# Kernel tuning notes

Measured on AMD Instinct MI355X. Metric: run time of the kernel, lower is better.

The kernel has to match this reference:

```python
import jax, jax.numpy as jnp
import numpy as np

N = 100000   # num_nodes
E = 300000   # num_edges
R = 200      # num_rels
B = 32       # num_bases (bdd blocks)
H = 128      # h_dim
SI = H // B  # submat_in = 4


def setup_inputs() -> dict:
    key = jax.random.key(0)
    ks = jax.random.split(key, 10)
    return {
        "node_ids": jnp.arange(N, dtype=jnp.int32),
        "src": jax.random.randint(ks[0], (E,), 0, N, dtype=jnp.int32),
        "dst": jax.random.randint(ks[1], (E,), 0, N, dtype=jnp.int32),
        "etypes": jax.random.randint(ks[2], (E,), 0, R, dtype=jnp.int32),
        "norm": jax.random.uniform(ks[3], (E, 1), dtype=jnp.float32),
        "emb": jax.random.normal(ks[4], (N, H), dtype=jnp.float32) * 0.02,
        "W1": jax.random.normal(ks[5], (R, B, SI, SI), dtype=jnp.float32) / np.float32(np.sqrt(SI)),
        "loop_w1": jax.random.normal(ks[6], (H, H), dtype=jnp.float32) / np.float32(np.sqrt(H)),
        "bias1": jnp.zeros((H,), dtype=jnp.float32),
        "W2": jax.random.normal(ks[7], (R, B, SI, 2 * SI), dtype=jnp.float32) / np.float32(np.sqrt(SI)),
        "loop_w2": jax.random.normal(ks[8], (H, 2 * H), dtype=jnp.float32) / np.float32(np.sqrt(H)),
        "bias2": jnp.zeros((2 * H,), dtype=jnp.float32),
        "eps": jax.random.normal(ks[9], (N, H), dtype=jnp.float32),
    }


def rel_graph_conv_bdd(h, src, dst, etypes, norm, W, loop_w, bias):
    """DGL RelGraphConv with regularizer='bdd', self_loop=True, bias=True."""
    _, Bb, si, so = W.shape
    h_src = h[src].reshape(-1, Bb, si)                  # (E, B, si)
    We = W[etypes]                                      # (E, B, si, so) gathered block weights
    msg = jnp.einsum('ebi,ebio->ebo', h_src, We).reshape(-1, Bb * so)  # (E, out)
    msg = msg * norm                                    # edge norm
    agg = jax.ops.segment_sum(msg, dst, num_segments=N)  # scatter-add to dst
    return agg + bias + h @ loop_w


def reference(node_ids, src, dst, etypes, norm, emb, W1, loop_w1, bias1, W2, loop_w2, bias2, eps):
    h = emb[node_ids]                                   # embedding lookup (N, H)
    h = jax.nn.relu(rel_graph_conv_bdd(h, src, dst, etypes, norm, W1, loop_w1, bias1))
    h = rel_graph_conv_bdd(h, src, dst, etypes, norm, W2, loop_w2, bias2)  # (N, 2H)
    # utils.gaussian_parameters: split last dim, v = softplus + 1e-8
    m, h_pre = jnp.split(h, 2, axis=-1)
    v = jax.nn.softplus(h_pre) + 1e-8
    # utils.sample_gaussian: reparameterized sample
    z = m + jnp.sqrt(v) * eps
    return z
```

## Files before the change

kernel.cpp:

```cpp
#include <hip/hip_runtime.h>
#include <math.h>

#define HD 128

union F4 { float4 v; float f[4]; };

typedef __attribute__((ext_vector_type(8))) short bf8_t;
typedef __attribute__((ext_vector_type(4))) float f4_t;

__device__ __forceinline__ float dot4(const F4& a, const F4& b){
  return fmaf(a.f[0], b.f[0], fmaf(a.f[1], b.f[1], fmaf(a.f[2], b.f[2], a.f[3]*b.f[3])));
}

__device__ __forceinline__ unsigned short f2bf(float f){
  unsigned int u = __float_as_uint(f);
  return (unsigned short)((u + 0x7fffu + ((u>>16)&1u)) >> 16);
}

__global__ void k_count(const int* __restrict__ dst, int* __restrict__ counts, int E){
  int e = blockIdx.x*256 + threadIdx.x;
  if (e < E) atomicAdd(&counts[dst[e]], 1);
}

__global__ void k_scan_block(const int* __restrict__ counts, int* __restrict__ scanTmp,
                             int* __restrict__ blockSums, int n){
  __shared__ int sm[256];
  int i = blockIdx.x*256 + threadIdx.x;
  int v = (i<n)?counts[i]:0;
  sm[threadIdx.x]=v; __syncthreads();
  for (int ofs=1; ofs<256; ofs<<=1){
    int t = (threadIdx.x>=ofs)?sm[threadIdx.x-ofs]:0;
    __syncthreads();
    sm[threadIdx.x]+=t;
    __syncthreads();
  }
  if (i<n) scanTmp[i]=sm[threadIdx.x];
  if (threadIdx.x==255) blockSums[blockIdx.x]=sm[255];
}

__global__ void k_scan_top(int* __restrict__ blockSums, int nb){
  __shared__ int sm[1024];
  int v = ((int)threadIdx.x<nb)?blockSums[threadIdx.x]:0;
  sm[threadIdx.x]=v; __syncthreads();
  for (int ofs=1; ofs<1024; ofs<<=1){
    int t = ((int)threadIdx.x>=ofs)?sm[threadIdx.x-ofs]:0;
    __syncthreads();
    sm[threadIdx.x]+=t;
    __syncthreads();
  }
  if ((int)threadIdx.x<nb) blockSums[threadIdx.x] = sm[threadIdx.x]-v;
}

__global__ void k_scan_fin(const int* __restrict__ scanTmp, const int* __restrict__ blockSums,
                           const int* __restrict__ counts,
                           int* __restrict__ row_ptr, int* __restrict__ cursors, int n){
  int i = blockIdx.x*256 + threadIdx.x;
  if (i<n){
    int incl = scanTmp[i] + blockSums[blockIdx.x];
    row_ptr[i+1] = incl;
    cursors[i] = incl - counts[i];
  }
  if (i==0) row_ptr[0]=0;
}

__global__ void k_scatter(const int* __restrict__ dst, const int* __restrict__ src,
                          const int* __restrict__ et, const float* __restrict__ norm,
                          int* __restrict__ cursors, int4* __restrict__ pay, int E){
  int e = blockIdx.x*256 + threadIdx.x;
  if (e<E){
    int p = atomicAdd(&cursors[dst[e]],1);
    pay[p] = make_int4(src[e], et[e], __float_as_int(norm[e]), 0);
  }
}

__global__ void k_w1t(const float* __restrict__ W, float* __restrict__ WT, int n){
  int d = blockIdx.x*256 + threadIdx.x;
  if (d < n){
    int i = d & 3, o = (d>>2) & 3, rb = d>>4;
    WT[d] = W[rb*16 + i*4 + o];
  }
}
__global__ void k_w2t(const float* __restrict__ W, float* __restrict__ WT, int n){
  int d = blockIdx.x*256 + threadIdx.x;
  if (d < n){
    int i = d & 3, o = (d>>2) & 7, rb = d>>5;
    WT[d] = W[rb*32 + i*8 + o];
  }
}

__global__ void k_wpack(const float* __restrict__ W, unsigned short* __restrict__ Wp,
                        int NCT, int NO){
  int t = blockIdx.x*256 + threadIdx.x;
  if (t >= NCT*256) return;
  int lane = t & 63, ks = (t>>6) & 3, ct = t >> 8;
  int k0 = ks*32 + (lane>>4)*8, col = ct*16 + (lane&15);
  unsigned short v[8];
  #pragma unroll
  for (int j=0;j<8;++j) v[j] = f2bf(W[(k0+j)*NO + col]);
  ushort4* dst = (ushort4*)&Wp[(size_t)t*8];
  dst[0] = make_ushort4(v[0],v[1],v[2],v[3]);
  dst[1] = make_ushort4(v[4],v[5],v[6],v[7]);
}

__global__ void k_gather(const int* __restrict__ ids, const float4* __restrict__ emb4,
                         float4* __restrict__ h0, unsigned short* __restrict__ h0b, int nf4){
  int i = blockIdx.x*256+threadIdx.x;
  if (i<nf4){
    int row = i>>5, c = i&31;
    float4 v = emb4[ids[row]*32 + c];
    h0[i] = v;
    *(ushort4*)&h0b[(size_t)i*4] = make_ushort4(f2bf(v.x),f2bf(v.y),f2bf(v.z),f2bf(v.w));
  }
}

__global__ __launch_bounds__(256)
void k_edge1(const int* __restrict__ row_ptr, const int4* __restrict__ pay,
             const float* __restrict__ h, const float* __restrict__ WT,
             float* __restrict__ agg, int Nn){
  int wid = (blockIdx.x*256 + threadIdx.x)>>6;
  wid = __builtin_amdgcn_readfirstlane(wid);
  int lane = threadIdx.x & 63;
  if (wid >= Nn) return;
  int e0 = row_ptr[wid], e1 = row_ptr[wid+1];
  int b0 = lane>>2, o = lane&3;
  float acc0=0.f, acc1=0.f;
  for (int e=e0; e<e1; e+=2){
    int4 p0 = pay[e];
    bool has2 = (e+1 < e1);
    int4 p1 = has2 ? pay[e+1] : p0;
    float n0 = __int_as_float(p0.z);
    float n1 = has2 ? __int_as_float(p1.z) : 0.f;
    const float* ha = &h[p0.x*HD];  const float* wa = &WT[p0.y*512];
    const float* hb = &h[p1.x*HD];  const float* wb = &WT[p1.y*512];
    F4 hA0,hB0,wA0,wB0,hA1,hB1,wA1,wB1;
    hA0.v = *(const float4*)&ha[b0*4];
    hB0.v = *(const float4*)&ha[(b0+16)*4];
    wA0.v = *(const float4*)&wa[b0*16 + o*4];
    wB0.v = *(const float4*)&wa[(b0+16)*16 + o*4];
    hA1.v = *(const float4*)&hb[b0*4];
    hB1.v = *(const float4*)&hb[(b0+16)*4];
    wA1.v = *(const float4*)&wb[b0*16 + o*4];
    wB1.v = *(const float4*)&wb[(b0+16)*16 + o*4];
    acc0 = fmaf(n0, dot4(hA0,wA0), acc0);
    acc1 = fmaf(n0, dot4(hB0,wB0), acc1);
    acc0 = fmaf(n1, dot4(hA1,wA1), acc0);
    acc1 = fmaf(n1, dot4(hB1,wB1), acc1);
  }
  agg[wid*HD + lane]      = acc0;
  agg[wid*HD + 64 + lane] = acc1;
}

__global__ __launch_bounds__(256)
void k_edge2(const int* __restrict__ row_ptr, const int4* __restrict__ pay,
             const float* __restrict__ h, const float* __restrict__ WT,
             float* __restrict__ agg, int Nn){
  int wid = (blockIdx.x*256 + threadIdx.x)>>6;
  wid = __builtin_amdgcn_readfirstlane(wid);
  int lane = threadIdx.x & 63;
  if (wid >= Nn) return;
  int e0 = row_ptr[wid], e1 = row_ptr[wid+1];
  int ob = lane>>3, o = lane&7;
  float acc[4] = {0.f,0.f,0.f,0.f};
  for (int e=e0; e<e1; e+=2){
    int4 p0 = pay[e];
    bool has2 = (e+1 < e1);
    int4 p1 = has2 ? pay[e+1] : p0;
    float n0 = __int_as_float(p0.z);
    float n1 = has2 ? __int_as_float(p1.z) : 0.f;
    const float* ha = &h[p0.x*HD];  const float* wa = &WT[p0.y*1024];
    const float* hb = &h[p1.x*HD];  const float* wb = &WT[p1.y*1024];
    F4 hva[4], wva[4], hvb[4], wvb[4];
    #pragma unroll
    for (int u=0; u<4; ++u){
      int b = ob + 8*u;
      hva[u].v = *(const float4*)&ha[b*4];
      wva[u].v = *(const float4*)&wa[b*32 + o*4];
      hvb[u].v = *(const float4*)&hb[b*4];
      wvb[u].v = *(const float4*)&wb[b*32 + o*4];
    }
    #pragma unroll
    for (int u=0; u<4; ++u){
      acc[u] = fmaf(n0, dot4(hva[u],wva[u]), acc[u]);
      acc[u] = fmaf(n1, dot4(hvb[u],wvb[u]), acc[u]);
    }
  }
  #pragma unroll
  for (int u=0; u<4; ++u) agg[wid*256 + u*64 + lane] = acc[u];
}

__global__ __launch_bounds__(256)
void k_mfma_relu(const unsigned short* __restrict__ Ab, const unsigned short* __restrict__ Wp,
                 const float* __restrict__ agg, const float* __restrict__ bias,
                 float* __restrict__ out, unsigned short* __restrict__ outb, int M){
  const int lane = threadIdx.x & 63;
  const int rowBase = blockIdx.x*64 + (threadIdx.x>>6)*16;
  const int ar = lane & 15, kg = lane >> 4;
  const int aclamp = min(rowBase + ar, M-1);
  f4_t acc[8];
  #pragma unroll
  for (int ct=0; ct<8; ++ct) acc[ct] = (f4_t)0.f;
  #pragma unroll
  for (int ks=0; ks<4; ++ks){
    bf8_t a = *(const bf8_t*)&Ab[(size_t)aclamp*HD + ks*32 + kg*8];
    #pragma unroll
    for (int ct=0; ct<8; ++ct){
      bf8_t b = *(const bf8_t*)&Wp[(size_t)((ct*4 + ks)*64 + lane)*8];
      acc[ct] = __builtin_amdgcn_mfma_f32_16x16x32_bf16(a, b, acc[ct], 0,0,0);
    }
  }
  const int crow = rowBase + kg*4;
  #pragma unroll
  for (int r=0; r<4; ++r){
    int gr = crow + r;
    if (gr >= M) continue;
    #pragma unroll
    for (int ct=0; ct<8; ++ct){
      int col = ct*16 + ar;
      float v = fmaxf(acc[ct][r] + agg[(size_t)gr*128 + col] + bias[col], 0.f);
      out[(size_t)gr*128 + col] = v;
      outb[(size_t)gr*128 + col] = f2bf(v);
    }
  }
}

__global__ __launch_bounds__(256)
void k_mfma_gauss(const unsigned short* __restrict__ Ab, const unsigned short* __restrict__ Wp,
                  const float* __restrict__ agg, const float* __restrict__ bias,
                  const float* __restrict__ eps, float* __restrict__ out, int M){
  const int lane = threadIdx.x & 63;
  const int bx = blockIdx.x & 1;
  const int rowBase = (blockIdx.x>>1)*64 + (threadIdx.x>>6)*16;
  const int ar = lane & 15, kg = lane >> 4;
  const int aclamp = min(rowBase + ar, M-1);
  f4_t accm[4], acch[4];
  #pragma unroll
  for (int ct=0; ct<4; ++ct){ accm[ct] = (f4_t)0.f; acch[ct] = (f4_t)0.f; }
  #pragma unroll
  for (int ks=0; ks<4; ++ks){
    bf8_t a = *(const bf8_t*)&Ab[(size_t)aclamp*HD + ks*32 + kg*8];
    #pragma unroll
    for (int ct=0; ct<4; ++ct){
      int ctm = bx*4 + ct, cth = 8 + bx*4 + ct;
      bf8_t bm = *(const bf8_t*)&Wp[(size_t)((ctm*4 + ks)*64 + lane)*8];
      bf8_t bh = *(const bf8_t*)&Wp[(size_t)((cth*4 + ks)*64 + lane)*8];
      accm[ct] = __builtin_amdgcn_mfma_f32_16x16x32_bf16(a, bm, accm[ct], 0,0,0);
      acch[ct] = __builtin_amdgcn_mfma_f32_16x16x32_bf16(a, bh, acch[ct], 0,0,0);
    }
  }
  const int crow = rowBase + kg*4;
  #pragma unroll
  for (int r=0; r<4; ++r){
    int gr = crow + r;
    if (gr >= M) continue;
    #pragma unroll
    for (int ct=0; ct<4; ++ct){
      int colm = bx*64 + ct*16 + ar;
      float m  = accm[ct][r] + agg[(size_t)gr*256 + colm]       + bias[colm];
      float hp = acch[ct][r] + agg[(size_t)gr*256 + colm + 128] + bias[colm+128];
      float sp = fmaxf(hp, 0.f) + log1pf(expf(-fabsf(hp)));
      out[(size_t)gr*128 + colm] = fmaf(sqrtf(sp + 1e-8f), eps[(size_t)gr*128 + colm], m);
    }
  }
}

extern "C" void kernel_launch(void* const* d_in, const int* in_sizes, int n_in,
                              void* d_out, int out_size, void* d_ws, size_t ws_size,
                              hipStream_t stream){
  (void)n_in; (void)out_size; (void)ws_size;
  const int*   node_ids = (const int*)d_in[0];
  const int*   src  = (const int*)d_in[1];
  const int*   dst  = (const int*)d_in[2];
  const int*   et   = (const int*)d_in[3];
  const float* norm = (const float*)d_in[4];
  const float* emb  = (const float*)d_in[5];
  const float* W1   = (const float*)d_in[6];
  const float* lw1  = (const float*)d_in[7];
  const float* b1   = (const float*)d_in[8];
  const float* W2   = (const float*)d_in[9];
  const float* lw2  = (const float*)d_in[10];
  const float* b2   = (const float*)d_in[11];
  const float* eps  = (const float*)d_in[12];
  float* out = (float*)d_out;

  const int N  = in_sizes[0];
  const int E  = in_sizes[1];
  const int n1 = in_sizes[6];
  const int n2 = in_sizes[9];

  char* w = (char*)d_ws;
  size_t szNH = (size_t)N*HD*sizeof(float);
  float* h0   = (float*)(w);
  float* agg2 = (float*)(w);
  float* h1   = (float*)(w + 2*szNH);
  float* agg1 = (float*)(w + 3*szNH);
  char*  ip   = w + 4*szNH;
  int4*  pay       = (int4*)ip;
  int*   counts    = (int*)(pay + E);
  int*   scanTmp   = counts + N;
  int*   row_ptr   = scanTmp + N;
  int*   cursors   = row_ptr + (N+1);
  int*   blockSums = cursors + N;
  float* W1T       = (float*)(blockSums + 1024);
  float* W2T       = W1T + n1;
  size_t tail      = ((size_t)((char*)(W2T + n2) - w) + 63) & ~(size_t)63;
  unsigned short* W1p = (unsigned short*)(w + tail);
  unsigned short* W2p = W1p + 8*256*8;
  unsigned short* h0b = W2p + 16*256*8;
  unsigned short* h1b = h0b + (size_t)N*HD;

  hipMemsetAsync(counts, 0, (size_t)N*sizeof(int), stream);

  int nb_e    = (E+255)/256;
  int nb_scan = (N+255)/256;

  k_w1t<<<(n1+255)/256, 256, 0, stream>>>(W1, W1T, n1);
  k_w2t<<<(n2+255)/256, 256, 0, stream>>>(W2, W2T, n2);
  k_wpack<<<8, 256, 0, stream>>>(lw1, W1p, 8, 128);
  k_wpack<<<16, 256, 0, stream>>>(lw2, W2p, 16, 256);
  k_gather<<<(N*32+255)/256, 256, 0, stream>>>(node_ids, (const float4*)emb, (float4*)h0, h0b, N*32);
  k_count<<<nb_e, 256, 0, stream>>>(dst, counts, E);
  k_scan_block<<<nb_scan, 256, 0, stream>>>(counts, scanTmp, blockSums, N);
  k_scan_top<<<1, 1024, 0, stream>>>(blockSums, nb_scan);
  k_scan_fin<<<nb_scan, 256, 0, stream>>>(scanTmp, blockSums, counts, row_ptr, cursors, N);
  k_scatter<<<nb_e, 256, 0, stream>>>(dst, src, et, norm, cursors, pay, E);

  int nb_rows = (N+3)/4;
  int nb_m    = (N+63)/64;

  k_edge1<<<nb_rows, 256, 0, stream>>>(row_ptr, pay, h0, W1T, agg1, N);
  k_mfma_relu<<<nb_m, 256, 0, stream>>>(h0b, W1p, agg1, b1, h1, h1b, N);
  k_edge2<<<nb_rows, 256, 0, stream>>>(row_ptr, pay, h1, W2T, agg2, N);
  k_mfma_gauss<<<nb_m*2, 256, 0, stream>>>(h1b, W2p, agg2, b2, eps, out, N);
}
```

Baseline: 430.5 us.

## Fuse prep kernels, store relation weights in bf16, remap edge kernels per block

Merges the embedding gather, in-degree count, per-relation weight transposes and self-loop weight packing into one launch, cutting five kernel launches. The per-relation block-diagonal weights are now stored as bf16, halving weight gather traffic in the edge kernels. The edge kernels are remapped so each lane owns one 4-wide input block and computes all of that block's outputs. The two half-wavefronts take alternate edges, with one payload prefetched ahead, and their partial sums are merged by a cross-half shuffle before a vectorized store. The bf16 weights add rounding error to the message computation, and the new mapping leaves half the lanes idle on nodes with a single in-edge.

```diff
diff --git a/kernel.cpp b/kernel.cpp
--- a/kernel.cpp
+++ b/kernel.cpp
@@ -7,19 +7,66 @@
 
 typedef __attribute__((ext_vector_type(8))) short bf8_t;
 typedef __attribute__((ext_vector_type(4))) float f4_t;
-
-__device__ __forceinline__ float dot4(const F4& a, const F4& b){
-  return fmaf(a.f[0], b.f[0], fmaf(a.f[1], b.f[1], fmaf(a.f[2], b.f[2], a.f[3]*b.f[3])));
-}
 
 __device__ __forceinline__ unsigned short f2bf(float f){
   unsigned int u = __float_as_uint(f);
   return (unsigned short)((u + 0x7fffu + ((u>>16)&1u)) >> 16);
 }
 
-__global__ void k_count(const int* __restrict__ dst, int* __restrict__ counts, int E){
-  int e = blockIdx.x*256 + threadIdx.x;
-  if (e < E) atomicAdd(&counts[dst[e]], 1);
+__device__ __forceinline__ float dotbf(const F4& h, unsigned int ua, unsigned int ub){
+  float w0 = __uint_as_float(ua << 16);
+  float w1 = __uint_as_float(ua & 0xffff0000u);
+  float w2 = __uint_as_float(ub << 16);
+  float w3 = __uint_as_float(ub & 0xffff0000u);
+  return fmaf(h.f[0], w0, fmaf(h.f[1], w1, fmaf(h.f[2], w2, h.f[3]*w3)));
+}
+
+__device__ __forceinline__ void wpack_one(const float* __restrict__ W,
+                                          unsigned short* __restrict__ Wp, int t, int NO){
+  int lane = t & 63, ks = (t>>6) & 3, ct = t >> 8;
+  int k0 = ks*32 + (lane>>4)*8, col = ct*16 + (lane&15);
+  unsigned short v[8];
+  #pragma unroll
+  for (int j=0;j<8;++j) v[j] = f2bf(W[(k0+j)*NO + col]);
+  ushort4* dst = (ushort4*)&Wp[(size_t)t*8];
+  dst[0] = make_ushort4(v[0],v[1],v[2],v[3]);
+  dst[1] = make_ushort4(v[4],v[5],v[6],v[7]);
+}
+
+__global__ void k_prep(const int* __restrict__ ids, const float4* __restrict__ emb4,
+                       float4* __restrict__ h0, unsigned short* __restrict__ h0b,
+                       const int* __restrict__ dst, int* __restrict__ counts,
+                       const float* __restrict__ W1, unsigned short* __restrict__ W1Tb,
+                       const float* __restrict__ W2, unsigned short* __restrict__ W2Tb,
+                       const float* __restrict__ lw1, unsigned short* __restrict__ W1p,
+                       const float* __restrict__ lw2, unsigned short* __restrict__ W2p,
+                       int NG, int E, int n1, int n2){
+  int i = blockIdx.x*256 + threadIdx.x;
+  if (i < NG){
+    int row = i>>5, c = i&31;
+    float4 v = emb4[ids[row]*32 + c];
+    h0[i] = v;
+    *(ushort4*)&h0b[(size_t)i*4] = make_ushort4(f2bf(v.x),f2bf(v.y),f2bf(v.z),f2bf(v.w));
+    return;
+  }
+  i -= NG;
+  if (i < E){ atomicAdd(&counts[dst[i]], 1); return; }
+  i -= E;
+  if (i < n1){
+    int ii = i & 3, o = (i>>2) & 3, rb = i>>4;
+    W1Tb[i] = f2bf(W1[rb*16 + ii*4 + o]);
+    return;
+  }
+  i -= n1;
+  if (i < n2){
+    int ii = i & 3, o = (i>>2) & 7, rb = i>>5;
+    W2Tb[i] = f2bf(W2[rb*32 + ii*8 + o]);
+    return;
+  }
+  i -= n2;
+  if (i < 2048){ wpack_one(lw1, W1p, i, 128); return; }
+  i -= 2048;
+  if (i < 4096){ wpack_one(lw2, W2p, i, 256); }
 }
 
 __global__ void k_scan_block(const int* __restrict__ counts, int* __restrict__ scanTmp,
@@ -73,119 +120,79 @@
   }
 }
 
-__global__ void k_w1t(const float* __restrict__ W, float* __restrict__ WT, int n){
-  int d = blockIdx.x*256 + threadIdx.x;
-  if (d < n){
-    int i = d & 3, o = (d>>2) & 3, rb = d>>4;
-    WT[d] = W[rb*16 + i*4 + o];
-  }
-}
-__global__ void k_w2t(const float* __restrict__ W, float* __restrict__ WT, int n){
-  int d = blockIdx.x*256 + threadIdx.x;
-  if (d < n){
-    int i = d & 3, o = (d>>2) & 7, rb = d>>5;
-    WT[d] = W[rb*32 + i*8 + o];
-  }
-}
-
-__global__ void k_wpack(const float* __restrict__ W, unsigned short* __restrict__ Wp,
-                        int NCT, int NO){
-  int t = blockIdx.x*256 + threadIdx.x;
-  if (t >= NCT*256) return;
-  int lane = t & 63, ks = (t>>6) & 3, ct = t >> 8;
-  int k0 = ks*32 + (lane>>4)*8, col = ct*16 + (lane&15);
-  unsigned short v[8];
-  #pragma unroll
-  for (int j=0;j<8;++j) v[j] = f2bf(W[(k0+j)*NO + col]);
-  ushort4* dst = (ushort4*)&Wp[(size_t)t*8];
-  dst[0] = make_ushort4(v[0],v[1],v[2],v[3]);
-  dst[1] = make_ushort4(v[4],v[5],v[6],v[7]);
-}
-
-__global__ void k_gather(const int* __restrict__ ids, const float4* __restrict__ emb4,
-                         float4* __restrict__ h0, unsigned short* __restrict__ h0b, int nf4){
-  int i = blockIdx.x*256+threadIdx.x;
-  if (i<nf4){
-    int row = i>>5, c = i&31;
-    float4 v = emb4[ids[row]*32 + c];
-    h0[i] = v;
-    *(ushort4*)&h0b[(size_t)i*4] = make_ushort4(f2bf(v.x),f2bf(v.y),f2bf(v.z),f2bf(v.w));
-  }
-}
-
 __global__ __launch_bounds__(256)
 void k_edge1(const int* __restrict__ row_ptr, const int4* __restrict__ pay,
-             const float* __restrict__ h, const float* __restrict__ WT,
+             const float* __restrict__ h, const unsigned short* __restrict__ WTb,
              float* __restrict__ agg, int Nn){
-  int wid = (blockIdx.x*256 + threadIdx.x)>>6;
-  wid = __builtin_amdgcn_readfirstlane(wid);
-  int lane = threadIdx.x & 63;
+  int wid = __builtin_amdgcn_readfirstlane((blockIdx.x*256 + threadIdx.x)>>6);
   if (wid >= Nn) return;
-  int e0 = row_ptr[wid], e1 = row_ptr[wid+1];
-  int b0 = lane>>2, o = lane&3;
-  float acc0=0.f, acc1=0.f;
-  for (int e=e0; e<e1; e+=2){
-    int4 p0 = pay[e];
-    bool has2 = (e+1 < e1);
-    int4 p1 = has2 ? pay[e+1] : p0;
-    float n0 = __int_as_float(p0.z);
-    float n1 = has2 ? __int_as_float(p1.z) : 0.f;
-    const float* ha = &h[p0.x*HD];  const float* wa = &WT[p0.y*512];
-    const float* hb = &h[p1.x*HD];  const float* wb = &WT[p1.y*512];
-    F4 hA0,hB0,wA0,wB0,hA1,hB1,wA1,wB1;
-    hA0.v = *(const float4*)&ha[b0*4];
-    hB0.v = *(const float4*)&ha[(b0+16)*4];
-    wA0.v = *(const float4*)&wa[b0*16 + o*4];
-    wB0.v = *(const float4*)&wa[(b0+16)*16 + o*4];
-    hA1.v = *(const float4*)&hb[b0*4];
-    hB1.v = *(const float4*)&hb[(b0+16)*4];
-    wA1.v = *(const float4*)&wb[b0*16 + o*4];
-    wB1.v = *(const float4*)&wb[(b0+16)*16 + o*4];
-    acc0 = fmaf(n0, dot4(hA0,wA0), acc0);
-    acc1 = fmaf(n0, dot4(hB0,wB0), acc1);
-    acc0 = fmaf(n1, dot4(hA1,wA1), acc0);
-    acc1 = fmaf(n1, dot4(hB1,wB1), acc1);
-  }
-  agg[wid*HD + lane]      = acc0;
-  agg[wid*HD + 64 + lane] = acc1;
+  const int lane = threadIdx.x & 63;
+  const int half = lane >> 5, b = lane & 31;
+  const int e0 = row_ptr[wid], e1 = row_ptr[wid+1];
+  float a0=0.f, a1=0.f, a2=0.f, a3=0.f;
+  int e = e0 + half;
+  int4 p;
+  if (e < e1) p = pay[e];
+  for (; e < e1; e += 2){
+    int4 pn = (e+2 < e1) ? pay[e+2] : p;
+    float nm = __int_as_float(p.z);
+    F4 hv; hv.v = *(const float4*)&h[(size_t)p.x*HD + b*4];
+    const uint4* wq = (const uint4*)&WTb[(size_t)p.y*512 + b*16];
+    uint4 q0 = wq[0], q1 = wq[1];
+    a0 = fmaf(nm, dotbf(hv, q0.x, q0.y), a0);
+    a1 = fmaf(nm, dotbf(hv, q0.z, q0.w), a1);
+    a2 = fmaf(nm, dotbf(hv, q1.x, q1.y), a2);
+    a3 = fmaf(nm, dotbf(hv, q1.z, q1.w), a3);
+    p = pn;
+  }
+  a0 += __shfl_xor(a0, 32); a1 += __shfl_xor(a1, 32);
+  a2 += __shfl_xor(a2, 32); a3 += __shfl_xor(a3, 32);
+  if (half == 0){
+    F4 o; o.f[0]=a0; o.f[1]=a1; o.f[2]=a2; o.f[3]=a3;
+    *(float4*)&agg[(size_t)wid*128 + b*4] = o.v;
+  }
 }
 
 __global__ __launch_bounds__(256)
 void k_edge2(const int* __restrict__ row_ptr, const int4* __restrict__ pay,
-             const float* __restrict__ h, const float* __restrict__ WT,
+             const float* __restrict__ h, const unsigned short* __restrict__ WTb,
              float* __restrict__ agg, int Nn){
-  int wid = (blockIdx.x*256 + threadIdx.x)>>6;
-  wid = __builtin_amdgcn_readfirstlane(wid);
-  int lane = threadIdx.x & 63;
+  int wid = __builtin_amdgcn_readfirstlane((blockIdx.x*256 + threadIdx.x)>>6);
   if (wid >= Nn) return;
-  int e0 = row_ptr[wid], e1 = row_ptr[wid+1];
-  int ob = lane>>3, o = lane&7;
-  float acc[4] = {0.f,0.f,0.f,0.f};
-  for (int e=e0; e<e1; e+=2){
-    int4 p0 = pay[e];
-    bool has2 = (e+1 < e1);
-    int4 p1 = has2 ? pay[e+1] : p0;
-    float n0 = __int_as_float(p0.z);
-    float n1 = has2 ? __int_as_float(p1.z) : 0.f;
-    const float* ha = &h[p0.x*HD];  const float* wa = &WT[p0.y*1024];
-    const float* hb = &h[p1.x*HD];  const float* wb = &WT[p1.y*1024];
-    F4 hva[4], wva[4], hvb[4], wvb[4];
-    #pragma unroll
-    for (int u=0; u<4; ++u){
-      int b = ob + 8*u;
-      hva[u].v = *(const float4*)&ha[b*4];
-      wva[u].v = *(const float4*)&wa[b*32 + o*4];
-      hvb[u].v = *(const float4*)&hb[b*4];
-      wvb[u].v = *(const float4*)&wb[b*32 + o*4];
-    }
-    #pragma unroll
-    for (int u=0; u<4; ++u){
-      acc[u] = fmaf(n0, dot4(hva[u],wva[u]), acc[u]);
-      acc[u] = fmaf(n1, dot4(hvb[u],wvb[u]), acc[u]);
-    }
-  }
-  #pragma unroll
-  for (int u=0; u<4; ++u) agg[wid*256 + u*64 + lane] = acc[u];
+  const int lane = threadIdx.x & 63;
+  const int half = lane >> 5, b = lane & 31;
+  const int e0 = row_ptr[wid], e1 = row_ptr[wid+1];
+  float acc[8];
+  #pragma unroll
+  for (int o=0;o<8;++o) acc[o]=0.f;
+  int e = e0 + half;
+  int4 p;
+  if (e < e1) p = pay[e];
+  for (; e < e1; e += 2){
+    int4 pn = (e+2 < e1) ? pay[e+2] : p;
+    float nm = __int_as_float(p.z);
+    F4 hv; hv.v = *(const float4*)&h[(size_t)p.x*HD + b*4];
+    const uint4* wq = (const uint4*)&WTb[(size_t)p.y*1024 + b*32];
+    uint4 q0 = wq[0], q1 = wq[1], q2 = wq[2], q3 = wq[3];
+    acc[0] = fmaf(nm, dotbf(hv, q0.x, q0.y), acc[0]);
+    acc[1] = fmaf(nm, dotbf(hv, q0.z, q0.w), acc[1]);
+    acc[2] = fmaf(nm, dotbf(hv, q1.x, q1.y), acc[2]);
+    acc[3] = fmaf(nm, dotbf(hv, q1.z, q1.w), acc[3]);
+    acc[4] = fmaf(nm, dotbf(hv, q2.x, q2.y), acc[4]);
+    acc[5] = fmaf(nm, dotbf(hv, q2.z, q2.w), acc[5]);
+    acc[6] = fmaf(nm, dotbf(hv, q3.x, q3.y), acc[6]);
+    acc[7] = fmaf(nm, dotbf(hv, q3.z, q3.w), acc[7]);
+    p = pn;
+  }
+  #pragma unroll
+  for (int o=0;o<8;++o) acc[o] += __shfl_xor(acc[o], 32);
+  if (half == 0){
+    F4 o0, o1;
+    #pragma unroll
+    for (int j=0;j<4;++j){ o0.f[j]=acc[j]; o1.f[j]=acc[4+j]; }
+    *(float4*)&agg[(size_t)wid*256 + b*8]     = o0.v;
+    *(float4*)&agg[(size_t)wid*256 + b*8 + 4] = o1.v;
+  }
 }
 
 __global__ __launch_bounds__(256)
@@ -300,25 +307,24 @@
   int*   row_ptr   = scanTmp + N;
   int*   cursors   = row_ptr + (N+1);
   int*   blockSums = cursors + N;
-  float* W1T       = (float*)(blockSums + 1024);
-  float* W2T       = W1T + n1;
-  size_t tail      = ((size_t)((char*)(W2T + n2) - w) + 63) & ~(size_t)63;
-  unsigned short* W1p = (unsigned short*)(w + tail);
-  unsigned short* W2p = W1p + 8*256*8;
-  unsigned short* h0b = W2p + 16*256*8;
-  unsigned short* h1b = h0b + (size_t)N*HD;
+  size_t tail      = ((size_t)((char*)(blockSums + 1024) - w) + 63) & ~(size_t)63;
+  unsigned short* W1Tb = (unsigned short*)(w + tail);
+  unsigned short* W2Tb = W1Tb + n1;
+  unsigned short* W1p  = W2Tb + n2;
+  unsigned short* W2p  = W1p + 8*256*8;
+  unsigned short* h0b  = W2p + 16*256*8;
+  unsigned short* h1b  = h0b + (size_t)N*HD;
 
   hipMemsetAsync(counts, 0, (size_t)N*sizeof(int), stream);
 
+  const int NG = N*32;
+  const int Tprep = NG + E + n1 + n2 + 2048 + 4096;
   int nb_e    = (E+255)/256;
   int nb_scan = (N+255)/256;
 
-  k_w1t<<<(n1+255)/256, 256, 0, stream>>>(W1, W1T, n1);
-  k_w2t<<<(n2+255)/256, 256, 0, stream>>>(W2, W2T, n2);
-  k_wpack<<<8, 256, 0, stream>>>(lw1, W1p, 8, 128);
-  k_wpack<<<16, 256, 0, stream>>>(lw2, W2p, 16, 256);
-  k_gather<<<(N*32+255)/256, 256, 0, stream>>>(node_ids, (const float4*)emb, (float4*)h0, h0b, N*32);
-  k_count<<<nb_e, 256, 0, stream>>>(dst, counts, E);
+  k_prep<<<(Tprep+255)/256, 256, 0, stream>>>(node_ids, (const float4*)emb, (float4*)h0, h0b,
+                                              dst, counts, W1, W1Tb, W2, W2Tb,
+                                              lw1, W1p, lw2, W2p, NG, E, n1, n2);
   k_scan_block<<<nb_scan, 256, 0, stream>>>(counts, scanTmp, blockSums, N);
   k_scan_top<<<1, 1024, 0, stream>>>(blockSums, nb_scan);
   k_scan_fin<<<nb_scan, 256, 0, stream>>>(scanTmp, blockSums, counts, row_ptr, cursors, N);
@@ -327,8 +333,8 @@
   int nb_rows = (N+3)/4;
   int nb_m    = (N+63)/64;
 
-  k_edge1<<<nb_rows, 256, 0, stream>>>(row_ptr, pay, h0, W1T, agg1, N);
+  k_edge1<<<nb_rows, 256, 0, stream>>>(row_ptr, pay, h0, W1Tb, agg1, N);
   k_mfma_relu<<<nb_m, 256, 0, stream>>>(h0b, W1p, agg1, b1, h1, h1b, N);
-  k_edge2<<<nb_rows, 256, 0, stream>>>(row_ptr, pay, h1, W2T, agg2, N);
+  k_edge2<<<nb_rows, 256, 0, stream>>>(row_ptr, pay, h1, W2Tb, agg2, N);
   k_mfma_gauss<<<nb_m*2, 256, 0, stream>>>(h1b, W2p, agg2, b2, eps, out, N);
 }
```

New measurement: 435.4 us. No clear change (+1.1%).
